# Kernel optimization log

Hardware: AMD Instinct MI355X
Metric: run time of the kernel (lower is better)

Reference implementation:

```python
import jax, jax.numpy as jnp
import numpy as np
from jax import lax

SCORE_THRESH = 0.05
NMS_THRESH = 0.5
DET_PER_IMG = 100
K_PRE = 2048  # pre-NMS candidate cap (batched_nms is never run on N*C dense candidates)
BBOX_XFORM_CLIP = float(np.log(1000.0 / 16.0))
WX, WY, WW, WH = 10.0, 10.0, 5.0, 5.0


def _decode(reg, props):
    # reg: [N, C, 4] deltas, props: [N, 4] xyxy -> [N, C, 4] xyxy (torchvision BoxCoder.decode)
    w = props[:, 2] - props[:, 0]
    h = props[:, 3] - props[:, 1]
    cx = props[:, 0] + 0.5 * w
    cy = props[:, 1] + 0.5 * h
    dx = reg[..., 0] / WX
    dy = reg[..., 1] / WY
    dw = jnp.minimum(reg[..., 2] / WW, BBOX_XFORM_CLIP)
    dh = jnp.minimum(reg[..., 3] / WH, BBOX_XFORM_CLIP)
    pcx = dx * w[:, None] + cx[:, None]
    pcy = dy * h[:, None] + cy[:, None]
    pw = jnp.exp(dw) * w[:, None]
    ph = jnp.exp(dh) * h[:, None]
    return jnp.stack([pcx - 0.5 * pw, pcy - 0.5 * ph, pcx + 0.5 * pw, pcy + 0.5 * ph], axis=-1)


def _pairwise_iou(b):
    # b: [K, 4] -> [K, K]
    area = (b[:, 2] - b[:, 0]) * (b[:, 3] - b[:, 1])
    lt = jnp.maximum(b[:, None, :2], b[None, :, :2])
    rb = jnp.minimum(b[:, None, 2:], b[None, :, 2:])
    wh = jnp.clip(rb - lt, 0.0)
    inter = wh[..., 0] * wh[..., 1]
    return inter / (area[:, None] + area[None, :] - inter)


def _greedy_nms(iou, valid, thresh):
    # boxes assumed sorted by descending score; valid: [K] bool initial keep mask
    K = iou.shape[0]
    idx = jnp.arange(K)
    def body(i, keep):
        sup = (iou[i] > thresh) & (idx > i) & keep[i]
        return keep & (~sup)
    return lax.fori_loop(0, K, body, valid)


def _process_image(logits, reg, props, img_h, img_w):
    # logits: [N, C], reg: [N, 4C], props: [N, 4]
    N, C = logits.shape
    scores = jax.nn.softmax(logits, axis=-1)[:, 1:]          # [N, C-1] drop background
    boxes = _decode(reg.reshape(N, C, 4), props)[:, 1:]      # [N, C-1, 4]
    boxes = jnp.stack([
        jnp.clip(boxes[..., 0], 0.0, img_w),
        jnp.clip(boxes[..., 1], 0.0, img_h),
        jnp.clip(boxes[..., 2], 0.0, img_w),
        jnp.clip(boxes[..., 3], 0.0, img_h),
    ], axis=-1)
    labels = jnp.broadcast_to(jnp.arange(1, C), (N, C - 1))
    boxes = boxes.reshape(-1, 4)       # [M, 4], M = N*(C-1)
    scores = scores.reshape(-1)
    labels = labels.reshape(-1)
    wd = boxes[:, 2] - boxes[:, 0]
    ht = boxes[:, 3] - boxes[:, 1]
    valid = (scores > SCORE_THRESH) & (wd >= 1.0) & (ht >= 1.0)  # score thresh + remove_small_boxes
    masked = jnp.where(valid, scores, -1.0)
    top_s, top_i = lax.top_k(masked, K_PRE)
    tb = boxes[top_i]
    tl = labels[top_i]
    tvalid = top_s > SCORE_THRESH
    # batched_nms via per-class coordinate offsets
    off = tl.astype(tb.dtype) * (jnp.max(tb) + 1.0)
    keep = _greedy_nms(_pairwise_iou(tb + off[:, None]), tvalid, NMS_THRESH)
    ks = jnp.where(keep, top_s, -1.0)
    fs, fi = lax.top_k(ks, DET_PER_IMG)
    fvalid = fs > SCORE_THRESH
    out_boxes = jnp.where(fvalid[:, None], tb[fi], 0.0)
    out_scores = jnp.where(fvalid, fs, 0.0)
    out_labels = jnp.where(fvalid, tl[fi], -1)
    return out_boxes, out_scores, out_labels


def setup_inputs() -> dict:
    key = jax.random.key(0)
    k1, k2, k3 = jax.random.split(key, 3)
    B, N, C, H, W = 8, 4000, 91, 800, 800
    pts = jax.random.uniform(k1, (B, N, 2, 2), dtype=jnp.float32, minval=0.0, maxval=float(W))
    proposals = jnp.concatenate([pts.min(axis=2), pts.max(axis=2)], axis=-1)  # valid xyxy
    class_logits = jax.random.normal(k2, (B * N, C), dtype=jnp.float32)
    box_regression = 0.5 * jax.random.normal(k3, (B * N, 4 * C), dtype=jnp.float32)
    return {"class_logits": class_logits, "box_regression": box_regression,
            "proposals": proposals, "img_h": H, "img_w": W}


def reference(class_logits, box_regression, proposals, img_h, img_w):
    B, N, _ = proposals.shape
    C = class_logits.shape[-1]
    logits = class_logits.reshape(B, N, C)
    reg = box_regression.reshape(B, N, 4 * C)
    fn = lambda l, r, p: _process_image(l, r, p, float(img_h), float(img_w))
    boxes, scores, labels = jax.vmap(fn)(logits, reg, proposals)
    return boxes, scores, labels
```

## Files before the change

kernel.cpp:

```cpp
#include <hip/hip_runtime.h>
#include <stdint.h>

typedef unsigned int u32;
typedef unsigned long long u64;
typedef __attribute__((ext_vector_type(2))) unsigned long long u64x2;

#define BIMG 8
#define NPROP 4000
#define NCLS 91
#define CM1 90
#define MCAND (NPROP * CM1)
#define KPRE 2048
#define NBUCKET 4096
#define NREP 8
#define SELCAP 16384
#define DETS 100
#define WLCAP 2048
#define SCORE_T 0.05f
#define NMS_T 0.5f
#define BBOX_CLIP 4.135166556742356f

#define HISTREP_OFF ((size_t)0)
#define BCNTREP_OFF (HISTREP_OFF + (size_t)NREP * BIMG * NBUCKET * 4)
#define META_OFF    (BCNTREP_OFF + (size_t)NREP * BIMG * NBUCKET * 4)
#define ZERO_BYTES  (META_OFF + 4096)
#define START_OFF   (ZERO_BYTES)
#define HISTTOT_OFF (START_OFF + (size_t)BIMG * NBUCKET * 4)
#define STARTREP_OFF (HISTTOT_OFF + (size_t)BIMG * NBUCKET * 4)
#define SEL_OFF     (STARTREP_OFF + (size_t)NREP * BIMG * NBUCKET * 4)
#define TBOX_OFF    (SEL_OFF + (size_t)BIMG * SELCAP * 8)
#define TSB_OFF     (TBOX_OFF + (size_t)BIMG * KPRE * 16)
#define TSC_OFF     (TSB_OFF + (size_t)BIMG * KPRE * 16)
#define TLB_OFF     (TSC_OFF + (size_t)BIMG * KPRE * 4)
#define TVL_OFF     (TLB_OFF + (size_t)BIMG * KPRE * 4)
#define KEEP_OFF    (TVL_OFF + (size_t)BIMG * KPRE * 4)
#define WLIST_OFF   (KEEP_OFF + (size_t)BIMG * 32 * 8)
#define UNION_OFF   (WLIST_OFF + (size_t)BIMG * WLCAP * 4)
#define UNION_BYTES ((size_t)BIMG * MCAND * 4)
#define WS_NEED     (UNION_OFF + UNION_BYTES)

__device__ __forceinline__ void decode_clip(const float4 rg, const float w, const float h,
                                            const float cx, const float cy,
                                            const float fw, const float fh, float bx[4]) {
    float dx = rg.x / 10.0f;
    float dy = rg.y / 10.0f;
    float dw = fminf(rg.z / 5.0f, BBOX_CLIP);
    float dh = fminf(rg.w / 5.0f, BBOX_CLIP);
    float pcx = dx * w + cx;
    float pcy = dy * h + cy;
    float pw  = expf(dw) * w;
    float phh = expf(dh) * h;
    bx[0] = fminf(fmaxf(pcx - 0.5f * pw,  0.0f), fw);
    bx[1] = fminf(fmaxf(pcy - 0.5f * phh, 0.0f), fh);
    bx[2] = fminf(fmaxf(pcx + 0.5f * pw,  0.0f), fw);
    bx[3] = fminf(fmaxf(pcy + 0.5f * phh, 0.0f), fh);
}

__global__ __launch_bounds__(256) void k1_score_hist(
    const float* __restrict__ logits, const float* __restrict__ reg,
    const float* __restrict__ props, const int* __restrict__ imh, const int* __restrict__ imw,
    u32* __restrict__ histrep, u32* __restrict__ cand_ord) {
    const int lane = threadIdx.x & 63;
    const int pid = blockIdx.x * 4 + (threadIdx.x >> 6);
    if (pid >= BIMG * NPROP) return;
    const int img = pid / NPROP;
    const float fw = (float)imw[0], fh = (float)imh[0];
    const float* lrow = logits + (size_t)pid * NCLS;
    float v0 = lrow[lane];
    float v1 = (lane < 27) ? lrow[lane + 64] : -3.0e38f;
    float mx = fmaxf(v0, v1);
#pragma unroll
    for (int o = 32; o > 0; o >>= 1) mx = fmaxf(mx, __shfl_xor(mx, o));
    float es = expf(v0 - mx) + ((lane < 27) ? expf(v1 - mx) : 0.0f);
#pragma unroll
    for (int o = 32; o > 0; o >>= 1) es += __shfl_xor(es, o);
    const float thr = mx + logf(es) - 2.9967323f;
    float4 p = reinterpret_cast<const float4*>(props)[pid];
    const float w = p.z - p.x, h = p.w - p.y;
    const float cx = p.x + 0.5f * w, cy = p.y + 0.5f * h;
    const float4* rrow = reinterpret_cast<const float4*>(reg) + (size_t)pid * NCLS;
    const int n = pid - img * NPROP;
    u32* co = cand_ord + (size_t)img * MCAND + (size_t)n * CM1;
#pragma unroll
    for (int batch = 0; batch < 2; ++batch) {
        int ci = lane + batch * 64;
        if (ci < CM1) {
            int c = ci + 1;
            float l = lrow[c];
            u32 o = 0u;
            if (l > thr) {
                float sc = expf(l - mx) / es;
                float4 rg = rrow[c];
                float bx[4];
                decode_clip(rg, w, h, cx, cy, fw, fh, bx);
                bool valid = (sc > SCORE_T) && (bx[2] - bx[0] >= 1.0f) && (bx[3] - bx[1] >= 1.0f);
                if (valid) {
                    o = __float_as_uint(sc) | 0x80000000u;
                    u32 t = (u32)img * MCAND + (u32)n * CM1 + (u32)ci;
                    int rep = (int)((t >> 8) & (NREP - 1));
                    atomicAdd(&histrep[((size_t)rep * BIMG + img) * NBUCKET + (o >> 20)], 1u);
                }
            }
            co[ci] = o;
        }
    }
}

__global__ __launch_bounds__(256) void k2_scan(
    const u32* __restrict__ histrep, u32* __restrict__ histtot,
    u32* __restrict__ start, u32* __restrict__ startrep, u32* __restrict__ meta,
    u32* __restrict__ wlist) {
    const int img = blockIdx.x;
    const int td = threadIdx.x;
    const int lane = td & 63, wv = td >> 6;
    u32 cnt[16]; u32 tsum = 0;
#pragma unroll
    for (int k = 0; k < 16; ++k) {
        const int bk = NBUCKET - 1 - (td * 16 + k);
        u32 c = 0;
#pragma unroll
        for (int r = 0; r < NREP; ++r)
            c += histrep[((size_t)r * BIMG + img) * NBUCKET + bk];
        cnt[k] = c; tsum += c;
    }
    u32 inc = tsum;
#pragma unroll
    for (int o = 1; o < 64; o <<= 1) { u32 t = __shfl_up(inc, o); if (lane >= o) inc += t; }
    __shared__ u32 wsum[4];
    __shared__ u32 TbkS, Vs;
    if (td == 0) TbkS = 0u;
    if (lane == 63) wsum[wv] = inc;
    __syncthreads();
    u32 wbase = 0;
    for (int i = 0; i < wv; ++i) wbase += wsum[i];
    if (td == 255) Vs = wbase + inc;
    const u32 excl0 = wbase + inc - tsum;
    u32 excl = excl0;
#pragma unroll
    for (int k = 0; k < 16; ++k) {
        const int bk = NBUCKET - 1 - (td * 16 + k);
        const u32 c = cnt[k];
        start[img * NBUCKET + bk] = excl;
        histtot[img * NBUCKET + bk] = c;
        u32 sub = excl;
#pragma unroll
        for (int r = 0; r < NREP; ++r) {
            startrep[((size_t)r * BIMG + img) * NBUCKET + bk] = sub;
            sub += histrep[((size_t)r * BIMG + img) * NBUCKET + bk];
        }
        if (c > 0 && excl < KPRE && excl + c >= KPRE) TbkS = (u32)bk;
        excl += c;
    }
    u32 qcnt = 0;
    {
        u32 e = excl0;
#pragma unroll
        for (int k = 0; k < 16; ++k) { if (cnt[k] >= 2 && e < KPRE) ++qcnt; e += cnt[k]; }
    }
    u32 qinc = qcnt;
#pragma unroll
    for (int o = 1; o < 64; o <<= 1) { u32 t = __shfl_up(qinc, o); if (lane >= o) qinc += t; }
    __shared__ u32 qws[4];
    if (lane == 63) qws[wv] = qinc;
    __syncthreads();
    u32 qbase = 0;
    for (int i = 0; i < wv; ++i) qbase += qws[i];
    u32 qoff = qbase + qinc - qcnt;
    {
        u32 e = excl0;
#pragma unroll
        for (int k = 0; k < 16; ++k) {
            const int bk = NBUCKET - 1 - (td * 16 + k);
            if (cnt[k] >= 2 && e < KPRE && qoff < WLCAP) wlist[img * WLCAP + (qoff++)] = (u32)bk;
            e += cnt[k];
        }
    }
    if (td == 255) meta[img * 8 + 3] = qbase + qinc;
    __syncthreads();
    if (td == 0) {
        u32 V = Vs;
        meta[img * 8 + 0] = V;
        meta[img * 8 + 1] = TbkS;
        meta[img * 8 + 2] = (V < KPRE) ? (KPRE - V) : 0u;
    }
}

__global__ __launch_bounds__(256) void k3_compact(
    const u32* __restrict__ cand_ord, const u32* __restrict__ startrep,
    const u32* __restrict__ meta, u32* __restrict__ bcntrep, u64* __restrict__ sel) {
    const u32 t = blockIdx.x * 256 + threadIdx.x;
    const int rep = (int)(blockIdx.x & (NREP - 1));
    if (t < (u32)(BIMG * MCAND)) {
        const int img = t / MCAND;
        const u32 idx = t - (u32)img * MCAND;
        const u32 o = cand_ord[t];
        if (o) {
            const u32 bk = o >> 20;
            if (bk >= meta[img * 8 + 1]) {
                const size_t ri = ((size_t)rep * BIMG + img) * NBUCKET + bk;
                const u32 pos = startrep[ri] + atomicAdd(&bcntrep[ri], 1u);
                if (pos < SELCAP)
                    sel[(size_t)img * SELCAP + pos] = ((u64)o << 32) | (u32)(~idx);
            }
        }
    }
    if (blockIdx.x < BIMG && threadIdx.x < 64) {
        const int img = blockIdx.x;
        const u32 need = meta[img * 8 + 2];
        if (need != 0) {
            const u32 V = meta[img * 8 + 0];
            const int lane = threadIdx.x;
            const u32 ORDN1 = 0x407FFFFFu;
            u32 filled = 0;
            for (u32 b0 = 0; b0 < MCAND && filled < need; b0 += 64) {
                u32 idx = b0 + (u32)lane;
                bool inv = (idx < MCAND) && (cand_ord[(size_t)img * MCAND + idx] == 0u);
                u64 bal = __ballot(inv);
                u32 pre = (u32)__popcll(bal & ((1ull << lane) - 1ull));
                if (inv && (filled + pre) < need)
                    sel[(size_t)img * SELCAP + V + filled + pre] =
                        ((u64)ORDN1 << 32) | (u32)(~idx);
                filled += (u32)__popcll(bal);
            }
        }
    }
}

__global__ __launch_bounds__(256) void k4_sortseg(
    const u32* __restrict__ histtot, const u32* __restrict__ start,
    const u32* __restrict__ meta, const u32* __restrict__ wlist, u64* __restrict__ sel) {
    __shared__ u64 arr[4096];
    const int img = blockIdx.y;
    const int tid = threadIdx.x;
    const u32 wcount = meta[img * 8 + 3];
    for (u32 wi = blockIdx.x; wi < wcount; wi += gridDim.x) {
        const u32 bk = (wi < WLCAP) ? wlist[img * WLCAP + wi] : 0u;
        u32 cnt = histtot[img * NBUCKET + bk];
        u32 st = start[img * NBUCKET + bk];
        if (cnt < 2 || st >= KPRE) continue;
        if (st + cnt > SELCAP) cnt = SELCAP - st;
        if (cnt > 4096) cnt = 4096;
        int n = 1;
        while (n < (int)cnt) n <<= 1;
        u64* seg = sel + (size_t)img * SELCAP + st;
        for (int i = tid; i < n; i += 256) arr[i] = (i < (int)cnt) ? seg[i] : 0ull;
        __syncthreads();
        for (int k = 2; k <= n; k <<= 1)
            for (int j = k >> 1; j > 0; j >>= 1) {
                for (int i = tid; i < n; i += 256) {
                    int ixj = i ^ j;
                    if (ixj > i) {
                        u64 a = arr[i], b = arr[ixj];
                        bool swp = ((i & k) == 0) ? (a < b) : (a > b);
                        if (swp) { arr[i] = b; arr[ixj] = a; }
                    }
                }
                __syncthreads();
            }
        for (int i = tid; i < (int)cnt; i += 256) seg[i] = arr[i];
        __syncthreads();
    }
}

__global__ __launch_bounds__(256) void k5_gather(
    const u64* __restrict__ sel, const float* __restrict__ reg, const float* __restrict__ props,
    const int* __restrict__ imh, const int* __restrict__ imw,
    float* __restrict__ tbox, float* __restrict__ tsb, float* __restrict__ tsc,
    int* __restrict__ tlb, u32* __restrict__ tvl) {
    const int img = blockIdx.x;
    const int tid = threadIdx.x;
    const float fw = (float)imw[0], fh = (float)imh[0];
    float bx[8][4];
    int lab[8];
    float lm = -3.0e38f;
#pragma unroll
    for (int t = 0; t < 8; ++t) {
        int s = t * 256 + tid;
        u64 key = sel[(size_t)img * SELCAP + s];
        u32 o = (u32)(key >> 32);
        u32 idx = ~((u32)key);
        u32 b = (o & 0x80000000u) ? (o & 0x7FFFFFFFu) : ~o;
        float sc = __uint_as_float(b);
        u32 n = idx / CM1;
        int c = (int)(idx - n * CM1) + 1;
        int pid = img * NPROP + (int)n;
        float4 p = reinterpret_cast<const float4*>(props)[pid];
        float w = p.z - p.x, h = p.w - p.y;
        float cx = p.x + 0.5f * w, cy = p.y + 0.5f * h;
        float4 rg = reinterpret_cast<const float4*>(reg)[(size_t)pid * NCLS + c];
        decode_clip(rg, w, h, cx, cy, fw, fh, bx[t]);
        lab[t] = c;
        lm = fmaxf(lm, fmaxf(fmaxf(bx[t][0], bx[t][1]), fmaxf(bx[t][2], bx[t][3])));
        reinterpret_cast<float4*>(tbox)[(size_t)img * KPRE + s] =
            make_float4(bx[t][0], bx[t][1], bx[t][2], bx[t][3]);
        tsc[(size_t)img * KPRE + s] = sc;
        tlb[(size_t)img * KPRE + s] = c;
        tvl[(size_t)img * KPRE + s] = (sc > SCORE_T) ? 1u : 0u;
    }
#pragma unroll
    for (int o2 = 32; o2 > 0; o2 >>= 1) lm = fmaxf(lm, __shfl_xor(lm, o2));
    __shared__ float wm[4];
    if ((tid & 63) == 0) wm[tid >> 6] = lm;
    __syncthreads();
    float mplus = fmaxf(fmaxf(wm[0], wm[1]), fmaxf(wm[2], wm[3])) + 1.0f;
#pragma unroll
    for (int t = 0; t < 8; ++t) {
        int s = t * 256 + tid;
        float off = (float)lab[t] * mplus;
        reinterpret_cast<float4*>(tsb)[(size_t)img * KPRE + s] =
            make_float4(bx[t][0] + off, bx[t][1] + off, bx[t][2] + off, bx[t][3] + off);
    }
}

__global__ __launch_bounds__(64) void k6_mask(
    const float* __restrict__ tsb, u64* __restrict__ mask) {
    const int img = blockIdx.z;
    const int tid = threadIdx.x;
    if (blockIdx.x < blockIdx.y) {
        const int i = blockIdx.y * 64 + tid;
        mask[((size_t)img * KPRE + i) * 32 + blockIdx.x] = 0ull;
        return;
    }
    const int j0 = blockIdx.x * 64;
    const int i0 = blockIdx.y * 64;
    __shared__ float4 cb[64];
    __shared__ float ca[64];
    float4 c = reinterpret_cast<const float4*>(tsb)[(size_t)img * KPRE + j0 + tid];
    cb[tid] = c;
    ca[tid] = (c.z - c.x) * (c.w - c.y);
    __syncthreads();
    const int i = i0 + tid;
    float4 r = reinterpret_cast<const float4*>(tsb)[(size_t)img * KPRE + i];
    float ra = (r.z - r.x) * (r.w - r.y);
    u64 bits = 0ull;
#pragma unroll 8
    for (int jj = 0; jj < 64; ++jj) {
        int j = j0 + jj;
        float4 cc = cb[jj];
        float wv = fmaxf(fminf(r.z, cc.z) - fmaxf(r.x, cc.x), 0.0f);
        float hv = fmaxf(fminf(r.w, cc.w) - fmaxf(r.y, cc.y), 0.0f);
        float inter = wv * hv;
        float iou = inter / ((ra + ca[jj]) - inter);
        if ((iou > NMS_T) && (j > i)) bits |= (1ull << jj);
    }
    mask[((size_t)img * KPRE + i) * 32 + (j0 >> 6)] = bits;
}

__device__ __forceinline__ u64 rdlane64(u64 v, int l) {
    u32 lo = (u32)__builtin_amdgcn_readlane((int)(u32)v, l);
    u32 hi = (u32)__builtin_amdgcn_readlane((int)(u32)(v >> 32), l);
    return ((u64)hi << 32) | lo;
}

__device__ __forceinline__ void g2l16(const void* g, void* l) {
    __builtin_amdgcn_global_load_lds(
        (const __attribute__((address_space(1))) void*)g,
        (__attribute__((address_space(3))) void*)l, 16, 0, 0);
}

__global__ __launch_bounds__(64) void k7_nms_sel(
    const u64* __restrict__ mask, const u32* __restrict__ tvl,
    const float* __restrict__ tsc, const float* __restrict__ tbox,
    const int* __restrict__ tlb, float* __restrict__ out) {
    __shared__ u64 smem[4096];
    const int img = blockIdx.x;
    const int lane = threadIdx.x;
    const int lg = lane >> 4;
    const u64* mrow = mask + (size_t)img * KPRE * 32;

    u64 accx = 0ull, accy = 0ull, rp = 0ull;
    for (int w = 0; w < 32; ++w) {
        bool tv = tvl[(size_t)img * KPRE + w * 64 + lane] != 0u;
        u64 iw = ~__ballot(tv);
        if (w == 0) rp = iw;
        if ((lane & 15) == (w >> 1)) { if (w & 1) accy = iw; else accx = iw; }
    }

    {
        const char* gsrc = (const char*)mrow + (size_t)lane * 16;
#pragma unroll
        for (int t = 0; t < 16; ++t)
            g2l16(gsrc + (size_t)t * 1024, (char*)smem + (size_t)t * 1024);
    }
    u64 diag = mrow[(size_t)lane * 32];

    u32 tk = 0;
    int bcut = 31;

#pragma unroll 1
    for (int b = 0; b < 32; ++b) {
        const size_t base32 = (size_t)b * 2048;
        const u64* cbuf = smem + (size_t)(b & 1) * 2048;

        u64 diagn = 0ull;
        if (b + 1 < 32) {
            diagn = mrow[base32 + 2048 + (size_t)lane * 32 + (b + 1)];
            const char* gsrc = (const char*)(mrow + base32 + 2048) + (size_t)lane * 16;
            char* nb_l = (char*)(smem + (size_t)((b + 1) & 1) * 2048);
#pragma unroll
            for (int t = 0; t < 16; ++t)
                g2l16(gsrc + (size_t)t * 1024, nb_l + (size_t)t * 1024);
        }

        u64 A = rp;
#pragma unroll
        for (int u = 0; u < 64; ++u) {
            u64 row = rdlane64(diag, u);
            if (!((A >> u) & 1ull)) A |= row;
        }
        const u64 keptw = ~A;

        if (b + 1 < 32) asm volatile("s_waitcnt vmcnt(17)" ::: "memory");
        else            asm volatile("s_waitcnt vmcnt(0)" ::: "memory");

#define LDV(K) u64x2 v##K = *(const u64x2*)&cbuf[128 * (K) + 2 * lane];
#define PRV(K) { u32 nib = (u32)(keptw >> (4 * (K))) & 15u; \
                 u32 kb = (nib >> lg) & 1u; \
                 accx |= kb ? v##K.x : 0ull; accy |= kb ? v##K.y : 0ull; }
        LDV(0) LDV(1) LDV(2) LDV(3)
        LDV(4) LDV(5) LDV(6) LDV(7)     PRV(0) PRV(1) PRV(2) PRV(3)
        LDV(8) LDV(9) LDV(10) LDV(11)   PRV(4) PRV(5) PRV(6) PRV(7)
        LDV(12) LDV(13) LDV(14) LDV(15) PRV(8) PRV(9) PRV(10) PRV(11)
        PRV(12) PRV(13) PRV(14) PRV(15)
#undef LDV
#undef PRV

        tk += (u32)__popcll(keptw);
        if (tk >= (u32)DETS) { bcut = b; break; }

        const int nb2 = b + 1;
        if (nb2 < 32) {
            u64 asel = (nb2 & 1) ? accy : accx;
            const int sl = (nb2 >> 1) & 15;
            rp = rdlane64(asel, sl) | rdlane64(asel, sl + 16) |
                 rdlane64(asel, sl + 32) | rdlane64(asel, sl + 48);
        }
        diag = diagn;
    }

    asm volatile("s_waitcnt vmcnt(0)" ::: "memory");

    accx |= __shfl_xor(accx, 16); accx |= __shfl_xor(accx, 32);
    accy |= __shfl_xor(accy, 16); accy |= __shfl_xor(accy, 32);

    u64 mxv = __shfl(accx, (lane >> 1) & 15);
    u64 myv = __shfl(accy, (lane >> 1) & 15);
    u64 kw = (lane & 1) ? ~myv : ~mxv;
    if (lane >= 32 || lane > bcut) kw = 0ull;

    u32 cnt = (u32)__popcll(kw);
    u32 inc = cnt;
#pragma unroll
    for (int o = 1; o < 64; o <<= 1) { u32 t = __shfl_up(inc, o); if (lane >= o) inc += t; }
    const u32 excl = inc - cnt;
    const u32 total = (u32)__shfl(inc, 63);

    float* ob0 = out + (size_t)img * DETS * 4;
    float* os0 = out + (size_t)BIMG * DETS * 4 + (size_t)img * DETS;
    float* ol0 = out + (size_t)BIMG * DETS * 5 + (size_t)img * DETS;

#pragma unroll
    for (int t = 0; t < 2; ++t) {
        u32 r = (u32)lane + (u32)t * 64;
        if (r < DETS && r >= total) {
            reinterpret_cast<float4*>(ob0)[r] = make_float4(0.f, 0.f, 0.f, 0.f);
            os0[r] = 0.0f;
            ol0[r] = -1.0f;
        }
    }
    u64 w = kw;
    u32 r = excl;
    while (w != 0ull && r < DETS) {
        int p = __ffsll((unsigned long long)w) - 1;
        w &= (w - 1ull);
        u32 s = (u32)lane * 64u + (u32)p;
        reinterpret_cast<float4*>(ob0)[r] =
            reinterpret_cast<const float4*>(tbox)[(size_t)img * KPRE + s];
        os0[r] = tsc[(size_t)img * KPRE + s];
        ol0[r] = (float)tlb[(size_t)img * KPRE + s];
        ++r;
    }
}

extern "C" void kernel_launch(void* const* d_in, const int* in_sizes, int n_in,
                              void* d_out, int out_size, void* d_ws, size_t ws_size,
                              hipStream_t stream) {
    const float* logits = (const float*)d_in[0];
    const float* reg    = (const float*)d_in[1];
    const float* props  = (const float*)d_in[2];
    const int*   imh    = (const int*)d_in[3];
    const int*   imw    = (const int*)d_in[4];
    float* out = (float*)d_out;
    char* ws = (char*)d_ws;
    if (ws_size < WS_NEED) return;

    u32* histrep  = (u32*)(ws + HISTREP_OFF);
    u32* bcntrep  = (u32*)(ws + BCNTREP_OFF);
    u32* meta     = (u32*)(ws + META_OFF);
    u32* start    = (u32*)(ws + START_OFF);
    u32* histtot  = (u32*)(ws + HISTTOT_OFF);
    u32* startrep = (u32*)(ws + STARTREP_OFF);
    u64* sel  = (u64*)(ws + SEL_OFF);
    float* tbox = (float*)(ws + TBOX_OFF);
    float* tsb  = (float*)(ws + TSB_OFF);
    float* tsc  = (float*)(ws + TSC_OFF);
    int*   tlb  = (int*)(ws + TLB_OFF);
    u32*   tvl  = (u32*)(ws + TVL_OFF);
    u32*   wlist = (u32*)(ws + WLIST_OFF);
    u32*   cand_ord = (u32*)(ws + UNION_OFF);
    u64*   mask = (u64*)(ws + UNION_OFF);

    hipMemsetAsync(d_ws, 0, ZERO_BYTES, stream);

    k1_score_hist<<<BIMG * NPROP / 4, 256, 0, stream>>>(logits, reg, props, imh, imw,
                                                        histrep, cand_ord);
    k2_scan<<<BIMG, 256, 0, stream>>>(histrep, histtot, start, startrep, meta, wlist);
    k3_compact<<<(BIMG * MCAND) / 256, 256, 0, stream>>>(cand_ord, startrep, meta, bcntrep, sel);
    k4_sortseg<<<dim3(64, BIMG), 256, 0, stream>>>(histtot, start, meta, wlist, sel);
    k5_gather<<<BIMG, 256, 0, stream>>>(sel, reg, props, imh, imw, tbox, tsb, tsc, tlb, tvl);
    k6_mask<<<dim3(32, 32, BIMG), 64, 0, stream>>>(tsb, mask);
    k7_nms_sel<<<BIMG, 64, 0, stream>>>(mask, tvl, tsc, tbox, tlb, out);
}
```

Measured before the change: 266.0 us.

## Compact valid candidates in scoring kernel, drop dense candidate array scan

The scoring kernel now appends valid candidates to per-image, per-replica lists through a wave-aggregated atomic, and writes a per-proposal validity bitmask instead of a dense 2.9M-entry order array. The compaction kernel then walks only the short lists rather than every candidate, and the padding path reads the bitmask. The segment sort gains a wave-level bitonic path for small buckets. Valid flags are passed to NMS as ballot words. Together these cut global memory traffic and the number of launched threads, at the cost of fixed-capacity lists that could overflow and a change in tie ordering within buckets.

```diff
diff --git a/kernel.cpp b/kernel.cpp
--- a/kernel.cpp
+++ b/kernel.cpp
@@ -14,6 +14,7 @@
 #define NBUCKET 4096
 #define NREP 8
 #define SELCAP 16384
+#define LSEG 16384
 #define DETS 100
 #define WLCAP 2048
 #define SCORE_T 0.05f
@@ -23,7 +24,8 @@
 #define HISTREP_OFF ((size_t)0)
 #define BCNTREP_OFF (HISTREP_OFF + (size_t)NREP * BIMG * NBUCKET * 4)
 #define META_OFF    (BCNTREP_OFF + (size_t)NREP * BIMG * NBUCKET * 4)
-#define ZERO_BYTES  (META_OFF + 4096)
+#define LCNT_OFF    (META_OFF + 4096)
+#define ZERO_BYTES  (LCNT_OFF + 256)
 #define START_OFF   (ZERO_BYTES)
 #define HISTTOT_OFF (START_OFF + (size_t)BIMG * NBUCKET * 4)
 #define STARTREP_OFF (HISTTOT_OFF + (size_t)BIMG * NBUCKET * 4)
@@ -32,12 +34,12 @@
 #define TSB_OFF     (TBOX_OFF + (size_t)BIMG * KPRE * 16)
 #define TSC_OFF     (TSB_OFF + (size_t)BIMG * KPRE * 16)
 #define TLB_OFF     (TSC_OFF + (size_t)BIMG * KPRE * 4)
-#define TVL_OFF     (TLB_OFF + (size_t)BIMG * KPRE * 4)
-#define KEEP_OFF    (TVL_OFF + (size_t)BIMG * KPRE * 4)
-#define WLIST_OFF   (KEEP_OFF + (size_t)BIMG * 32 * 8)
-#define UNION_OFF   (WLIST_OFF + (size_t)BIMG * WLCAP * 4)
-#define UNION_BYTES ((size_t)BIMG * MCAND * 4)
-#define WS_NEED     (UNION_OFF + UNION_BYTES)
+#define TVLB_OFF    (TLB_OFF + (size_t)BIMG * KPRE * 4)
+#define WLIST_OFF   (TVLB_OFF + (size_t)BIMG * 32 * 8)
+#define CLIST_OFF   (WLIST_OFF + (size_t)BIMG * WLCAP * 4)
+#define CVALID_OFF  (CLIST_OFF + (size_t)BIMG * NREP * LSEG * 8)
+#define MASK_OFF    (CVALID_OFF + (size_t)BIMG * NPROP * 2 * 8)
+#define WS_NEED     (MASK_OFF + (size_t)BIMG * KPRE * 32 * 8)
 
 __device__ __forceinline__ void decode_clip(const float4 rg, const float w, const float h,
                                             const float cx, const float cy,
@@ -59,7 +61,8 @@
 __global__ __launch_bounds__(256) void k1_score_hist(
     const float* __restrict__ logits, const float* __restrict__ reg,
     const float* __restrict__ props, const int* __restrict__ imh, const int* __restrict__ imw,
-    u32* __restrict__ histrep, u32* __restrict__ cand_ord) {
+    u32* __restrict__ histrep, u64* __restrict__ clist, u32* __restrict__ lcnt,
+    u64* __restrict__ cvalid) {
     const int lane = threadIdx.x & 63;
     const int pid = blockIdx.x * 4 + (threadIdx.x >> 6);
     if (pid >= BIMG * NPROP) return;
@@ -80,28 +83,44 @@
     const float cx = p.x + 0.5f * w, cy = p.y + 0.5f * h;
     const float4* rrow = reinterpret_cast<const float4*>(reg) + (size_t)pid * NCLS;
     const int n = pid - img * NPROP;
-    u32* co = cand_ord + (size_t)img * MCAND + (size_t)n * CM1;
+    const int rep = n & (NREP - 1);
+    const float sh0 = __shfl(v0, (lane + 1) & 63);
+    const float sh1 = __shfl(v1, (lane + 1) & 63);
 #pragma unroll
     for (int batch = 0; batch < 2; ++batch) {
-        int ci = lane + batch * 64;
+        const int ci = lane + batch * 64;
+        bool valid = false;
+        u32 ob = 0u;
         if (ci < CM1) {
-            int c = ci + 1;
-            float l = lrow[c];
-            u32 o = 0u;
+            const float l = (batch == 0) ? ((lane == 63) ? sh1 : sh0) : sh1;
             if (l > thr) {
                 float sc = expf(l - mx) / es;
-                float4 rg = rrow[c];
+                float4 rg = rrow[ci + 1];
                 float bx[4];
                 decode_clip(rg, w, h, cx, cy, fw, fh, bx);
-                bool valid = (sc > SCORE_T) && (bx[2] - bx[0] >= 1.0f) && (bx[3] - bx[1] >= 1.0f);
+                valid = (sc > SCORE_T) && (bx[2] - bx[0] >= 1.0f) && (bx[3] - bx[1] >= 1.0f);
                 if (valid) {
-                    o = __float_as_uint(sc) | 0x80000000u;
-                    u32 t = (u32)img * MCAND + (u32)n * CM1 + (u32)ci;
-                    int rep = (int)((t >> 8) & (NREP - 1));
-                    atomicAdd(&histrep[((size_t)rep * BIMG + img) * NBUCKET + (o >> 20)], 1u);
+                    ob = __float_as_uint(sc) | 0x80000000u;
+                    atomicAdd(&histrep[((size_t)rep * BIMG + img) * NBUCKET + (ob >> 20)], 1u);
                 }
             }
-            co[ci] = o;
+        }
+        const u64 bal = __ballot(valid);
+        if (lane == 0) cvalid[(size_t)pid * 2 + batch] = bal;
+        if (bal) {
+            const u32 cw = (u32)__popcll(bal);
+            const int leader = __ffsll((unsigned long long)bal) - 1;
+            u32 base = 0;
+            if (lane == leader) base = atomicAdd(&lcnt[img * NREP + rep], cw);
+            base = __shfl(base, leader);
+            if (valid) {
+                const u32 pre = (u32)__popcll(bal & ((1ull << lane) - 1ull));
+                const u32 pos = base + pre;
+                if (pos < LSEG) {
+                    const u32 idx = (u32)n * CM1 + (u32)ci;
+                    clist[((size_t)img * NREP + rep) * LSEG + pos] = ((u64)ob << 32) | (u32)(~idx);
+                }
+            }
         }
     }
 }
@@ -186,37 +205,41 @@
 }
 
 __global__ __launch_bounds__(256) void k3_compact(
-    const u32* __restrict__ cand_ord, const u32* __restrict__ startrep,
+    const u64* __restrict__ clist, const u32* __restrict__ lcnt,
+    const u64* __restrict__ cvalid, const u32* __restrict__ startrep,
     const u32* __restrict__ meta, u32* __restrict__ bcntrep, u64* __restrict__ sel) {
-    const u32 t = blockIdx.x * 256 + threadIdx.x;
-    const int rep = (int)(blockIdx.x & (NREP - 1));
-    if (t < (u32)(BIMG * MCAND)) {
-        const int img = t / MCAND;
-        const u32 idx = t - (u32)img * MCAND;
-        const u32 o = cand_ord[t];
-        if (o) {
-            const u32 bk = o >> 20;
-            if (bk >= meta[img * 8 + 1]) {
-                const size_t ri = ((size_t)rep * BIMG + img) * NBUCKET + bk;
-                const u32 pos = startrep[ri] + atomicAdd(&bcntrep[ri], 1u);
-                if (pos < SELCAP)
-                    sel[(size_t)img * SELCAP + pos] = ((u64)o << 32) | (u32)(~idx);
-            }
-        }
-    }
-    if (blockIdx.x < BIMG && threadIdx.x < 64) {
-        const int img = blockIdx.x;
+    const int img = blockIdx.z;
+    const int rep = blockIdx.y;
+    u32 cnt = lcnt[img * NREP + rep];
+    if (cnt > LSEG) cnt = LSEG;
+    const u32 cutoff = meta[img * 8 + 1];
+    for (u32 i = blockIdx.x * 256 + threadIdx.x; i < cnt; i += gridDim.x * 256) {
+        const u64 e = clist[((size_t)img * NREP + rep) * LSEG + i];
+        const u32 bk = (u32)(e >> 52);
+        if (bk >= cutoff) {
+            const size_t ri = ((size_t)rep * BIMG + img) * NBUCKET + bk;
+            const u32 pos = startrep[ri] + atomicAdd(&bcntrep[ri], 1u);
+            if (pos < SELCAP) sel[(size_t)img * SELCAP + pos] = e;
+        }
+    }
+    if (blockIdx.y == 0 && blockIdx.x == 0 && threadIdx.x < 64) {
         const u32 need = meta[img * 8 + 2];
         if (need != 0) {
             const u32 V = meta[img * 8 + 0];
-            const int lane = threadIdx.x;
+            const int lv = threadIdx.x;
             const u32 ORDN1 = 0x407FFFFFu;
             u32 filled = 0;
             for (u32 b0 = 0; b0 < MCAND && filled < need; b0 += 64) {
-                u32 idx = b0 + (u32)lane;
-                bool inv = (idx < MCAND) && (cand_ord[(size_t)img * MCAND + idx] == 0u);
-                u64 bal = __ballot(inv);
-                u32 pre = (u32)__popcll(bal & ((1ull << lane) - 1ull));
+                const u32 idx = b0 + (u32)lv;
+                bool inv = false;
+                if (idx < MCAND) {
+                    const u32 nn = (u32)(((u64)idx * 3054198967ull) >> 38);
+                    const u32 cq = idx - nn * 90u;
+                    const u64 wb = cvalid[((size_t)img * NPROP + nn) * 2 + (cq >> 6)];
+                    inv = ((wb >> (cq & 63)) & 1ull) == 0ull;
+                }
+                const u64 bal = __ballot(inv);
+                const u32 pre = (u32)__popcll(bal & ((1ull << lv) - 1ull));
                 if (inv && (filled + pre) < need)
                     sel[(size_t)img * SELCAP + V + filled + pre] =
                         ((u64)ORDN1 << 32) | (u32)(~idx);
@@ -237,7 +260,7 @@
         const u32 bk = (wi < WLCAP) ? wlist[img * WLCAP + wi] : 0u;
         u32 cnt = histtot[img * NBUCKET + bk];
         u32 st = start[img * NBUCKET + bk];
-        if (cnt < 2 || st >= KPRE) continue;
+        if (cnt <= 64 || st >= KPRE) continue;
         if (st + cnt > SELCAP) cnt = SELCAP - st;
         if (cnt > 4096) cnt = 4096;
         int n = 1;
@@ -260,13 +283,35 @@
         for (int i = tid; i < (int)cnt; i += 256) seg[i] = arr[i];
         __syncthreads();
     }
+    const int wv = tid >> 6, lane = tid & 63;
+    for (u32 wi = blockIdx.x * 4 + wv; wi < wcount; wi += gridDim.x * 4) {
+        const u32 bk = (wi < WLCAP) ? wlist[img * WLCAP + wi] : 0u;
+        u32 cnt = histtot[img * NBUCKET + bk];
+        u32 st = start[img * NBUCKET + bk];
+        if (cnt < 2 || cnt > 64 || st >= KPRE) continue;
+        if (st + cnt > SELCAP) cnt = SELCAP - st;
+        u64* seg = sel + (size_t)img * SELCAP + st;
+        u64 key = (lane < (int)cnt) ? seg[lane] : 0ull;
+#pragma unroll
+        for (int k = 2; k <= 64; k <<= 1) {
+#pragma unroll
+            for (int j = k >> 1; j > 0; j >>= 1) {
+                u64 other = __shfl_xor(key, j);
+                bool takeMax = ((lane & j) == 0) == ((lane & k) == 0);
+                u64 hi2 = (key > other) ? key : other;
+                u64 lo2 = (key > other) ? other : key;
+                key = takeMax ? hi2 : lo2;
+            }
+        }
+        if (lane < (int)cnt) seg[lane] = key;
+    }
 }
 
 __global__ __launch_bounds__(256) void k5_gather(
     const u64* __restrict__ sel, const float* __restrict__ reg, const float* __restrict__ props,
     const int* __restrict__ imh, const int* __restrict__ imw,
     float* __restrict__ tbox, float* __restrict__ tsb, float* __restrict__ tsc,
-    int* __restrict__ tlb, u32* __restrict__ tvl) {
+    int* __restrict__ tlb, u64* __restrict__ tvlb) {
     const int img = blockIdx.x;
     const int tid = threadIdx.x;
     const float fw = (float)imw[0], fh = (float)imh[0];
@@ -295,7 +340,8 @@
             make_float4(bx[t][0], bx[t][1], bx[t][2], bx[t][3]);
         tsc[(size_t)img * KPRE + s] = sc;
         tlb[(size_t)img * KPRE + s] = c;
-        tvl[(size_t)img * KPRE + s] = (sc > SCORE_T) ? 1u : 0u;
+        u64 bw = __ballot(sc > SCORE_T);
+        if ((tid & 63) == 0) tvlb[img * 32 + t * 4 + (tid >> 6)] = bw;
     }
 #pragma unroll
     for (int o2 = 32; o2 > 0; o2 >>= 1) lm = fmaxf(lm, __shfl_xor(lm, o2));
@@ -359,7 +405,7 @@
 }
 
 __global__ __launch_bounds__(64) void k7_nms_sel(
-    const u64* __restrict__ mask, const u32* __restrict__ tvl,
+    const u64* __restrict__ mask, const u64* __restrict__ tvlb,
     const float* __restrict__ tsc, const float* __restrict__ tbox,
     const int* __restrict__ tlb, float* __restrict__ out) {
     __shared__ u64 smem[4096];
@@ -368,12 +414,13 @@
     const int lg = lane >> 4;
     const u64* mrow = mask + (size_t)img * KPRE * 32;
 
-    u64 accx = 0ull, accy = 0ull, rp = 0ull;
-    for (int w = 0; w < 32; ++w) {
-        bool tv = tvl[(size_t)img * KPRE + w * 64 + lane] != 0u;
-        u64 iw = ~__ballot(tv);
-        if (w == 0) rp = iw;
-        if ((lane & 15) == (w >> 1)) { if (w & 1) accy = iw; else accx = iw; }
+    u64 accx, accy, rp;
+    {
+        u64 nv = 0ull;
+        if (lane < 32) nv = ~tvlb[img * 32 + lane];
+        rp   = __shfl(nv, 0);
+        accx = __shfl(nv, (lane & 15) * 2);
+        accy = __shfl(nv, (lane & 15) * 2 + 1);
     }
 
     {
@@ -497,6 +544,7 @@
     u32* histrep  = (u32*)(ws + HISTREP_OFF);
     u32* bcntrep  = (u32*)(ws + BCNTREP_OFF);
     u32* meta     = (u32*)(ws + META_OFF);
+    u32* lcnt     = (u32*)(ws + LCNT_OFF);
     u32* start    = (u32*)(ws + START_OFF);
     u32* histtot  = (u32*)(ws + HISTTOT_OFF);
     u32* startrep = (u32*)(ws + STARTREP_OFF);
@@ -505,19 +553,21 @@
     float* tsb  = (float*)(ws + TSB_OFF);
     float* tsc  = (float*)(ws + TSC_OFF);
     int*   tlb  = (int*)(ws + TLB_OFF);
-    u32*   tvl  = (u32*)(ws + TVL_OFF);
+    u64*   tvlb = (u64*)(ws + TVLB_OFF);
     u32*   wlist = (u32*)(ws + WLIST_OFF);
-    u32*   cand_ord = (u32*)(ws + UNION_OFF);
-    u64*   mask = (u64*)(ws + UNION_OFF);
+    u64*   clist = (u64*)(ws + CLIST_OFF);
+    u64*   cvalid = (u64*)(ws + CVALID_OFF);
+    u64*   mask = (u64*)(ws + MASK_OFF);
 
     hipMemsetAsync(d_ws, 0, ZERO_BYTES, stream);
 
     k1_score_hist<<<BIMG * NPROP / 4, 256, 0, stream>>>(logits, reg, props, imh, imw,
-                                                        histrep, cand_ord);
+                                                        histrep, clist, lcnt, cvalid);
     k2_scan<<<BIMG, 256, 0, stream>>>(histrep, histtot, start, startrep, meta, wlist);
-    k3_compact<<<(BIMG * MCAND) / 256, 256, 0, stream>>>(cand_ord, startrep, meta, bcntrep, sel);
+    k3_compact<<<dim3(4, NREP, BIMG), 256, 0, stream>>>(clist, lcnt, cvalid, startrep,
+                                                        meta, bcntrep, sel);
     k4_sortseg<<<dim3(64, BIMG), 256, 0, stream>>>(histtot, start, meta, wlist, sel);
-    k5_gather<<<BIMG, 256, 0, stream>>>(sel, reg, props, imh, imw, tbox, tsb, tsc, tlb, tvl);
+    k5_gather<<<BIMG, 256, 0, stream>>>(sel, reg, props, imh, imw, tbox, tsb, tsc, tlb, tvlb);
     k6_mask<<<dim3(32, 32, BIMG), 64, 0, stream>>>(tsb, mask);
-    k7_nms_sel<<<BIMG, 64, 0, stream>>>(mask, tvl, tsc, tbox, tlb, out);
-}
+    k7_nms_sel<<<BIMG, 64, 0, stream>>>(mask, tvlb, tsc, tbox, tlb, out);
+}
```

Result: slower. 606.4 us (+127.9%).
